# Kernel optimization log

Hardware: AMD Instinct MI355X
Metric: run time of the kernel (lower is better)

## Reference

```python
import jax, jax.numpy as jnp
import numpy as np

E = 1024   # embed_dim
H = 16     # num_heads
D = E // H # head dim = 64
NUM_BUCKETS = 32
MAX_DISTANCE = 128


def _relative_position_bucket(rel, num_buckets=NUM_BUCKETS, max_distance=MAX_DISTANCE):
    # T5-style bucketing (bidirectional): sign half + log-spaced far buckets.
    nb = num_buckets // 2
    buckets = (rel > 0).astype(jnp.int32) * nb
    rel = jnp.abs(rel)
    max_exact = nb // 2
    is_small = rel < max_exact
    # clamp to >=1 before log to avoid -inf on the masked-out branch
    rel_f = jnp.maximum(rel, 1).astype(jnp.float32)
    large = max_exact + (
        jnp.log(rel_f / max_exact) / np.log(max_distance / max_exact) * (nb - max_exact)
    ).astype(jnp.int32)
    large = jnp.minimum(large, nb - 1)
    return buckets + jnp.where(is_small, rel, large)


def setup_inputs() -> dict:
    key = jax.random.key(0)
    ks = jax.random.split(key, 6)
    B, S, K = 2, 2048, 2048
    w = 0.02
    return {
        "hidden_states": jax.random.normal(ks[0], (B, S, E), jnp.float32),
        "key_value_states": jax.random.normal(ks[1], (B, K, E), jnp.float32),
        "Wq": jax.random.normal(ks[2], (E, E), jnp.float32) * w,
        "Wkv": jax.random.normal(ks[3], (E, 2 * E), jnp.float32) * w,
        "Wo": jax.random.normal(ks[4], (E, E), jnp.float32) * w,
        "rel_bias": jax.random.normal(ks[5], (NUM_BUCKETS, H), jnp.float32) * w,
    }


def reference(hidden_states, key_value_states, Wq, Wkv, Wo, rel_bias):
    B, S, _ = hidden_states.shape
    K = key_value_states.shape[1]
    # projections (no bias, no 1/sqrt(d) scaling — T5 style)
    q = (hidden_states @ Wq).reshape(B, S, H, D).transpose(0, 2, 1, 3)      # [B,H,S,D]
    kv = (key_value_states @ Wkv).reshape(B, K, 2, H, D)
    k = kv[:, :, 0].transpose(0, 2, 1, 3)                                   # [B,H,K,D]
    v = kv[:, :, 1].transpose(0, 2, 1, 3)                                   # [B,H,K,D]
    scores = jnp.einsum('bhsd,bhkd->bhsk', q, k)                            # [B,H,S,K]
    # relative position bias
    rel = jnp.arange(K)[None, :] - jnp.arange(S)[:, None]                   # [S,K]
    buckets = _relative_position_bucket(rel)                                # [S,K]
    bias = rel_bias[buckets].transpose(2, 0, 1)[None]                       # [1,H,S,K]
    scores = scores + bias
    attn = jax.nn.softmax(scores.astype(jnp.float32), axis=-1).astype(scores.dtype)
    out = jnp.einsum('bhsk,bhkd->bshd', attn, v).reshape(B, S, E)
    return out @ Wo
```

## Files before the change

### kernel.cpp

```cpp
#include <hip/hip_runtime.h>
#include <hip/hip_bf16.h>
#include <math.h>

typedef __hip_bfloat16 bf16;
typedef __bf16 bf16x4 __attribute__((ext_vector_type(4)));
typedef __bf16 bf16x8 __attribute__((ext_vector_type(8)));
typedef float f32x4 __attribute__((ext_vector_type(4)));
typedef float f32x16 __attribute__((ext_vector_type(16)));
typedef unsigned short us4 __attribute__((ext_vector_type(4)));

#define LOG2E 1.44269504088896340736f

#if defined(__has_builtin)
#if __has_builtin(__builtin_amdgcn_exp2f)
#define EXP2(x) __builtin_amdgcn_exp2f(x)
#else
#define EXP2(x) exp2f(x)
#endif
#else
#define EXP2(x) exp2f(x)
#endif

__device__ inline __bf16 f2b(float f) {
  __hip_bfloat16 h = __float2bfloat16(f);
  return *reinterpret_cast<__bf16*>(&h);
}
__device__ inline unsigned short b2u(float f) {
  __hip_bfloat16 h = __float2bfloat16(f);
  return *reinterpret_cast<unsigned short*>(&h);
}
__device__ inline unsigned short b2u_fast(float f) {
  union { float f; unsigned u; } v;
  v.f = f;
  return (unsigned short)((v.u + 0x8000u) >> 16);
}
__device__ inline bf16x8 ld16(const bf16* p) {
  bf16x4 lo = *(const bf16x4*)p;
  bf16x4 hi = *(const bf16x4*)(p + 4);
  return __builtin_shufflevector(lo, hi, 0, 1, 2, 3, 4, 5, 6, 7);
}
__device__ inline void st16(bf16* p, uint4 v) {
  *(uint2*)p = make_uint2(v.x, v.y);
  *(uint2*)(p + 4) = make_uint2(v.z, v.w);
}
__device__ inline us4 shfl32_us4(us4 v) {
  uint2 u = *(uint2*)&v;
  u.x = __shfl_xor(u.x, 32);
  u.y = __shfl_xor(u.y, 32);
  return *(us4*)&u;
}
__device__ inline bf16x8 mk8(us4 lo, us4 hi) {
  bf16x4 l = *(bf16x4*)&lo;
  bf16x4 h = *(bf16x4*)&hi;
  return __builtin_shufflevector(l, h, 0, 1, 2, 3, 4, 5, 6, 7);
}
__device__ inline void async16(const bf16* g, bf16* l) {
  __builtin_amdgcn_global_load_lds(
      (const __attribute__((address_space(1))) unsigned int*)g,
      (__attribute__((address_space(3))) unsigned int*)l, 16, 0, 0);
}

__global__ void prep_k(const float* __restrict__ Wq, const float* __restrict__ Wkv,
                       const float* __restrict__ Wo, const float* __restrict__ rel_bias,
                       bf16* __restrict__ WqT, bf16* __restrict__ WkvT,
                       bf16* __restrict__ WoT, float* __restrict__ lut) {
  __shared__ float tile[32][33];
  int z = blockIdx.z;
  int tx = threadIdx.x, ty = threadIdx.y;
  if (z == 3) {
    if (blockIdx.y != 0 || blockIdx.x >= 16) return;
    int r = blockIdx.x * 256 + ty * 32 + tx;
    int rel = r - 2048;
    int bkt = rel > 0 ? 16 : 0;
    int ar = rel < 0 ? -rel : rel;
    int idx;
    if (ar < 8) {
      idx = bkt + ar;
    } else {
      double t = log((double)ar / 8.0) / log(16.0) * 8.0;
      int lg = 8 + (int)t;
      if (lg > 15) lg = 15;
      idx = bkt + lg;
    }
    for (int h = 0; h < 16; ++h)
      lut[h * 4096 + r] = rel_bias[idx * 16 + h] * LOG2E;
    return;
  }
  const float* in = z == 0 ? Wq : (z == 1 ? Wkv : Wo);
  bf16* out = z == 0 ? WqT : (z == 1 ? WkvT : WoT);
  int cols = z == 1 ? 2048 : 1024;
  int c0 = blockIdx.x * 32;
  if (c0 >= cols) return;
  int r0 = blockIdx.y * 32;
  for (int i = ty; i < 32; i += 8)
    tile[i][tx] = in[(size_t)(r0 + i) * cols + c0 + tx];
  __syncthreads();
  for (int i = ty; i < 32; i += 8)
    out[(size_t)(c0 + i) * 1024 + r0 + tx] = __float2bfloat16(tile[tx][i]);
}

__global__ __launch_bounds__(256) void gemm_qkv_k(const float* __restrict__ hf,
                                                  const float* __restrict__ kvf,
                                                  const bf16* __restrict__ WqT,
                                                  const bf16* __restrict__ WkvT,
                                                  bf16* __restrict__ Qb,
                                                  bf16* __restrict__ Kb,
                                                  bf16* __restrict__ Vt) {
  __shared__ __align__(16) bf16 As[128 * 32];
  __shared__ __align__(16) bf16 Bs[128 * 32];
  const int tid = threadIdx.x;
  const int lane = tid & 63;
  const int w = tid >> 6;
  const int wm = (w >> 1) * 64;
  const int wn = (w & 1) * 64;
  const int l15 = lane & 15;
  const int quad = lane >> 4;
  const int srow = lane >> 2;
  const int skg = lane & 3;

  const bool isQ = blockIdx.y < 8;
  const float* A = isQ ? hf : kvf;
  const bf16* Bt = isQ ? WqT : WkvT;
  const int n0 = (isQ ? blockIdx.y : blockIdx.y - 8) * 128;
  const int m0 = blockIdx.x * 128;
  const bool isV = (!isQ) && (n0 >= 1024);

  f32x4 acc[4][4];
#pragma unroll
  for (int i = 0; i < 4; ++i)
#pragma unroll
    for (int j = 0; j < 4; ++j) acc[i][j] = (f32x4){0.f, 0.f, 0.f, 0.f};

  for (int k0 = 0; k0 < 1024; k0 += 32) {
    __syncthreads();
#pragma unroll
    for (int rep = 0; rep < 2; ++rep) {
      int seg = w * 2 + rep;
      const float* src = A + (size_t)(m0 + seg * 16 + srow) * 1024 + k0 + skg * 8;
      float4 a0 = *(const float4*)src;
      float4 a1 = *(const float4*)(src + 4);
      bf16x8 v;
      v[0] = f2b(a0.x); v[1] = f2b(a0.y); v[2] = f2b(a0.z); v[3] = f2b(a0.w);
      v[4] = f2b(a1.x); v[5] = f2b(a1.y); v[6] = f2b(a1.z); v[7] = f2b(a1.w);
      st16(As + seg * 512 + lane * 8, *(uint4*)&v);
      async16(Bt + (size_t)(n0 + seg * 16 + srow) * 1024 + k0 + skg * 8, Bs + seg * 512);
    }
    __syncthreads();
    bf16x8 af[4], bfr[4];
#pragma unroll
    for (int i = 0; i < 4; ++i)
      af[i] = *(const bf16x8*)(As + (wm + i * 16 + l15) * 32 + quad * 8);
#pragma unroll
    for (int j = 0; j < 4; ++j)
      bfr[j] = *(const bf16x8*)(Bs + (wn + j * 16 + l15) * 32 + quad * 8);
    if (isV) {
#pragma unroll
      for (int i = 0; i < 4; ++i)
#pragma unroll
        for (int j = 0; j < 4; ++j)
          acc[i][j] = __builtin_amdgcn_mfma_f32_16x16x32_bf16(af[i], bfr[j], acc[i][j], 0, 0, 0);
    } else {
#pragma unroll
      for (int i = 0; i < 4; ++i)
#pragma unroll
        for (int j = 0; j < 4; ++j)
          acc[i][j] = __builtin_amdgcn_mfma_f32_16x16x32_bf16(bfr[j], af[i], acc[i][j], 0, 0, 0);
    }
  }

  if (isV) {
#pragma unroll
    for (int i = 0; i < 4; ++i) {
      int gmb = m0 + wm + i * 16 + quad * 4;
      int b = gmb >> 11, kp = gmb & 2047;
#pragma unroll
      for (int j = 0; j < 4; ++j) {
        int gn = n0 + wn + j * 16 + l15;
        int h = (gn >> 6) & 15, d = gn & 63;
        us4 pk;
#pragma unroll
        for (int r = 0; r < 4; ++r) pk[r] = b2u(acc[i][j][r]);
        *(us4*)(Vt + ((((size_t)b * 16 + h) * 64 + d) << 11) + kp) = pk;
      }
    }
    return;
  }
  const float scale = isQ ? LOG2E : 1.0f;
  bf16* dst = isQ ? Qb : Kb;
#pragma unroll
  for (int i = 0; i < 4; ++i) {
    int gm = m0 + wm + i * 16 + l15;
    int b = gm >> 11, s = gm & 2047;
#pragma unroll
    for (int j = 0; j < 4; ++j) {
      int gn = n0 + wn + j * 16 + quad * 4;
      int h = (gn >> 6) & 15, d0 = gn & 63;
      us4 pk;
#pragma unroll
      for (int r = 0; r < 4; ++r) pk[r] = b2u(acc[i][j][r] * scale);
      *(us4*)(dst + ((((size_t)b * 16 + h) * 2048 + s) << 6) + d0) = pk;
    }
  }
}

__global__ __launch_bounds__(256) void gemm_o_k(const bf16* __restrict__ A,
                                                const bf16* __restrict__ Bt,
                                                float* __restrict__ C0) {
  __shared__ __align__(16) bf16 As[128 * 32];
  __shared__ __align__(16) bf16 Bs[64 * 32];
  const int tid = threadIdx.x;
  const int lane = tid & 63;
  const int w = tid >> 6;
  const int wm = w * 32;
  const int m0 = blockIdx.x * 128;
  const int n0 = blockIdx.y * 64;
  const int l15 = lane & 15;
  const int quad = lane >> 4;
  const int srow = lane >> 2;
  const int skg = lane & 3;

  f32x4 acc[2][4];
#pragma unroll
  for (int i = 0; i < 2; ++i)
#pragma unroll
    for (int j = 0; j < 4; ++j) acc[i][j] = (f32x4){0.f, 0.f, 0.f, 0.f};

  for (int k0 = 0; k0 < 1024; k0 += 32) {
    __syncthreads();
#pragma unroll
    for (int rep = 0; rep < 2; ++rep) {
      int seg = w * 2 + rep;
      async16(A + (size_t)(m0 + seg * 16 + srow) * 1024 + k0 + skg * 8, As + seg * 512);
    }
    async16(Bt + (size_t)(n0 + w * 16 + srow) * 1024 + k0 + skg * 8, Bs + w * 512);
    __syncthreads();
    bf16x8 af[2], bfr[4];
#pragma unroll
    for (int i = 0; i < 2; ++i)
      af[i] = *(const bf16x8*)(As + (wm + i * 16 + l15) * 32 + quad * 8);
#pragma unroll
    for (int j = 0; j < 4; ++j)
      bfr[j] = *(const bf16x8*)(Bs + (j * 16 + l15) * 32 + quad * 8);
#pragma unroll
    for (int i = 0; i < 2; ++i)
#pragma unroll
      for (int j = 0; j < 4; ++j)
        acc[i][j] = __builtin_amdgcn_mfma_f32_16x16x32_bf16(bfr[j], af[i], acc[i][j], 0, 0, 0);
  }
#pragma unroll
  for (int i = 0; i < 2; ++i) {
    int gm = m0 + wm + i * 16 + l15;
#pragma unroll
    for (int j = 0; j < 4; ++j) {
      int gn = n0 + j * 16 + quad * 4;
      *(f32x4*)(C0 + (size_t)gm * 1024 + gn) = acc[i][j];
    }
  }
}

#define STK 68
#define SVK 136
#define KS_OFF 8704
#define VS_OFF 43520
__global__ __launch_bounds__(512, 4) void attn_k(const bf16* __restrict__ Qb,
                                                 const bf16* __restrict__ Kb,
                                                 const bf16* __restrict__ Vt,
                                                 const float* __restrict__ lut,
                                                 bf16* __restrict__ Ob) {
  __shared__ __align__(16) char smem[78336];
  float* lbias = (float*)smem;
  bf16* Ksb = (bf16*)(smem + KS_OFF);
  bf16* Vsb = (bf16*)(smem + VS_OFF);

  const int tid = threadIdx.x;
  const int lane = tid & 63;
  const int w = tid >> 6;
  const int wq = w & 3;
  const int kg = w >> 2;
  const int t256 = tid & 255;
  const int q31 = lane & 31;
  const int half = lane >> 5;

  bf16* Ks = Ksb + kg * (128 * STK);
  bf16* Vs = Vsb + kg * (64 * SVK);

  const int qt = blockIdx.x;
  const int bh = blockIdx.y;
  const int h = bh & 15, b = bh >> 4;
  const int qb = qt * 128;

  const int gbase = h * 4096 + 1921 - qb;
  for (int t = tid; t < 2175; t += 512) lbias[t] = lut[gbase + t];

  const size_t base = (size_t)bh * 2048 * 64;
  const size_t vbase = (size_t)bh * 64 * 2048;
  const int qg = qb + wq * 32 + q31;

  bf16x8 qf[4];
#pragma unroll
  for (int c = 0; c < 4; ++c)
    qf[c] = *(const bf16x8*)(Qb + base + (size_t)qg * 64 + c * 16 + half * 8);

  f32x16 oacc[2];
#pragma unroll
  for (int dj = 0; dj < 2; ++dj)
#pragma unroll
    for (int r = 0; r < 16; ++r) oacc[dj][r] = 0.f;
  float l_run = 0.f;

  const int kt0 = kg * 128;

  for (int it = 0; it < 8; ++it) {
    const int kt = it * 256 + kt0;
    __syncthreads();
    {
      uint4 kr[4], vr[4];
#pragma unroll
      for (int rep = 0; rep < 4; ++rep) {
        int slot = t256 + rep * 256;
        kr[rep] = *(const uint4*)(Kb + base + (size_t)(kt + (slot >> 3)) * 64 + (slot & 7) * 8);
        vr[rep] = *(const uint4*)(Vt + vbase + (size_t)(slot >> 4) * 2048 + kt + (slot & 15) * 8);
      }
#pragma unroll
      for (int rep = 0; rep < 4; ++rep) {
        int slot = t256 + rep * 256;
        st16(Ks + (slot >> 3) * STK + (slot & 7) * 8, kr[rep]);
        st16(Vs + (slot >> 4) * SVK + (slot & 15) * 8, vr[rep]);
      }
    }
    __syncthreads();

    const int xbase = kt + 127 + 4 * half - wq * 32 - q31;
#pragma unroll
    for (int mt = 0; mt < 4; ++mt) {
      f32x16 sacc;
#pragma unroll
      for (int a2 = 0; a2 < 4; ++a2)
#pragma unroll
        for (int rr = 0; rr < 4; ++rr)
          sacc[4 * a2 + rr] = lbias[xbase + mt * 32 + 8 * a2 + rr];
#pragma unroll
      for (int c = 0; c < 4; ++c) {
        bf16x8 kf = ld16(Ks + (mt * 32 + q31) * STK + c * 16 + half * 8);
        sacc = __builtin_amdgcn_mfma_f32_32x32x16_bf16(kf, qf[c], sacc, 0, 0, 0);
      }

      us4 ownq[4];
      f32x4 sv = (f32x4){0.f, 0.f, 0.f, 0.f};
#pragma unroll
      for (int a = 0; a < 4; ++a) {
        us4 pk;
#pragma unroll
        for (int rr = 0; rr < 4; ++rr) {
          float p = EXP2(sacc[4 * a + rr]);
          sv[rr] += p;
          pk[rr] = b2u_fast(p);
        }
        ownq[a] = pk;
      }
      l_run += (sv[0] + sv[1]) + (sv[2] + sv[3]);

      us4 rcv0 = shfl32_us4(half ? ownq[0] : ownq[1]);
      us4 rcv1 = shfl32_us4(half ? ownq[2] : ownq[3]);

#pragma unroll
      for (int p = 0; p < 2; ++p) {
        us4 rc = p ? rcv1 : rcv0;
        bf16x8 pfc = half ? mk8(rc, ownq[2 * p + 1]) : mk8(ownq[2 * p], rc);
#pragma unroll
        for (int dj = 0; dj < 2; ++dj) {
          bf16x8 vf = ld16(Vs + (dj * 32 + q31) * SVK + (mt * 2 + p) * 16 + half * 8);
          oacc[dj] = __builtin_amdgcn_mfma_f32_32x32x16_bf16(vf, pfc, oacc[dj], 0, 0, 0);
        }
      }
    }
  }

  l_run += __shfl_xor(l_run, 32);

  __syncthreads();
  float* mbuf = (float*)smem;
  if (kg) {
    float* p = mbuf + ((size_t)(wq * 64 + lane)) * 35;
    p[0] = l_run;
#pragma unroll
    for (int dj = 0; dj < 2; ++dj)
#pragma unroll
      for (int r = 0; r < 16; ++r) p[1 + dj * 16 + r] = oacc[dj][r];
  }
  __syncthreads();
  if (kg) return;

  const float* p = mbuf + ((size_t)(wq * 64 + lane)) * 35;
  float inv = 1.0f / (l_run + p[0]);

#pragma unroll
  for (int dj = 0; dj < 2; ++dj)
#pragma unroll
    for (int g = 0; g < 4; ++g) {
      us4 pk;
#pragma unroll
      for (int rr = 0; rr < 4; ++rr)
        pk[rr] = b2u((oacc[dj][4 * g + rr] + p[1 + dj * 16 + 4 * g + rr]) * inv);
      int d0 = dj * 32 + 8 * g + 4 * half;
      *(us4*)(Ob + ((size_t)(b * 2048 + qg)) * 1024 + h * 64 + d0) = pk;
    }
}

extern "C" void kernel_launch(void* const* d_in, const int* in_sizes, int n_in,
                              void* d_out, int out_size, void* d_ws, size_t ws_size,
                              hipStream_t stream) {
  const float* hidden = (const float*)d_in[0];
  const float* kvs    = (const float*)d_in[1];
  const float* Wq     = (const float*)d_in[2];
  const float* Wkv    = (const float*)d_in[3];
  const float* Wo     = (const float*)d_in[4];
  const float* relb   = (const float*)d_in[5];
  float* out = (float*)d_out;

  char* ws = (char*)d_ws;
  bf16* WqT  = (bf16*)(ws + (size_t)0);
  bf16* WkvT = (bf16*)(ws + ((size_t)2 << 20));
  bf16* WoT  = (bf16*)(ws + ((size_t)6 << 20));
  bf16* Ob   = (bf16*)(ws + ((size_t)8 << 20));
  bf16* Qb   = (bf16*)(ws + ((size_t)16 << 20));
  bf16* Kb   = (bf16*)(ws + ((size_t)24 << 20));
  bf16* Vt   = (bf16*)(ws + ((size_t)32 << 20));
  float* LUT = (float*)(ws + ((size_t)40 << 20));

  prep_k<<<dim3(64, 32, 4), dim3(32, 8), 0, stream>>>(Wq, Wkv, Wo, relb, WqT, WkvT, WoT, LUT);
  gemm_qkv_k<<<dim3(32, 24), 256, 0, stream>>>(hidden, kvs, WqT, WkvT, Qb, Kb, Vt);
  attn_k<<<dim3(16, 32), 512, 0, stream>>>(Qb, Kb, Vt, LUT, Ob);
  gemm_o_k<<<dim3(32, 16), 256, 0, stream>>>(Ob, WoT, out);
}
```

Measured before the change: 244.7 us.

## Register-prefetch next GEMM k-tile and pad LDS rows in projection GEMMs

Both projection GEMMs drop the direct global-to-LDS async loads. They now load the next k-slice into registers while MFMAs run on the current slice, then store it to LDS with a padded row stride of 36 to reduce bank conflicts on fragment reads. Launch bounds now request 3 blocks per SM. This software pipelining is meant to hide global latency, which the single-buffered loop previously exposed between the two syncs. In exchange it uses more registers and LDS, and the extra st16 ds writes replace the async path.

Measured after the change: 460.4 us. 1.88x slower.

```diff
diff --git a/kernel.cpp b/kernel.cpp
--- a/kernel.cpp
+++ b/kernel.cpp
@@ -53,11 +53,6 @@
   bf16x4 l = *(bf16x4*)&lo;
   bf16x4 h = *(bf16x4*)&hi;
   return __builtin_shufflevector(l, h, 0, 1, 2, 3, 4, 5, 6, 7);
-}
-__device__ inline void async16(const bf16* g, bf16* l) {
-  __builtin_amdgcn_global_load_lds(
-      (const __attribute__((address_space(1))) unsigned int*)g,
-      (__attribute__((address_space(3))) unsigned int*)l, 16, 0, 0);
 }
 
 __global__ void prep_k(const float* __restrict__ Wq, const float* __restrict__ Wkv,
@@ -99,15 +94,16 @@
     out[(size_t)(c0 + i) * 1024 + r0 + tx] = __float2bfloat16(tile[tx][i]);
 }
 
-__global__ __launch_bounds__(256) void gemm_qkv_k(const float* __restrict__ hf,
-                                                  const float* __restrict__ kvf,
-                                                  const bf16* __restrict__ WqT,
-                                                  const bf16* __restrict__ WkvT,
-                                                  bf16* __restrict__ Qb,
-                                                  bf16* __restrict__ Kb,
-                                                  bf16* __restrict__ Vt) {
-  __shared__ __align__(16) bf16 As[128 * 32];
-  __shared__ __align__(16) bf16 Bs[128 * 32];
+#define PS 36
+__global__ __launch_bounds__(256, 3) void gemm_qkv_k(const float* __restrict__ hf,
+                                                     const float* __restrict__ kvf,
+                                                     const bf16* __restrict__ WqT,
+                                                     const bf16* __restrict__ WkvT,
+                                                     bf16* __restrict__ Qb,
+                                                     bf16* __restrict__ Kb,
+                                                     bf16* __restrict__ Vt) {
+  __shared__ __align__(16) bf16 As[128 * PS];
+  __shared__ __align__(16) bf16 Bs[128 * PS];
   const int tid = threadIdx.x;
   const int lane = tid & 63;
   const int w = tid >> 6;
@@ -131,28 +127,42 @@
 #pragma unroll
     for (int j = 0; j < 4; ++j) acc[i][j] = (f32x4){0.f, 0.f, 0.f, 0.f};
 
-  for (int k0 = 0; k0 < 1024; k0 += 32) {
-    __syncthreads();
+  float4 pa[2][2];
+  uint4 pb[2];
+  auto LOAD = [&](int k0) {
 #pragma unroll
     for (int rep = 0; rep < 2; ++rep) {
       int seg = w * 2 + rep;
       const float* src = A + (size_t)(m0 + seg * 16 + srow) * 1024 + k0 + skg * 8;
-      float4 a0 = *(const float4*)src;
-      float4 a1 = *(const float4*)(src + 4);
+      pa[rep][0] = *(const float4*)src;
+      pa[rep][1] = *(const float4*)(src + 4);
+      pb[rep] = *(const uint4*)(Bt + (size_t)(n0 + seg * 16 + srow) * 1024 + k0 + skg * 8);
+    }
+  };
+  LOAD(0);
+
+  for (int k0 = 0; k0 < 1024; k0 += 32) {
+    __syncthreads();
+#pragma unroll
+    for (int rep = 0; rep < 2; ++rep) {
+      int seg = w * 2 + rep;
       bf16x8 v;
-      v[0] = f2b(a0.x); v[1] = f2b(a0.y); v[2] = f2b(a0.z); v[3] = f2b(a0.w);
-      v[4] = f2b(a1.x); v[5] = f2b(a1.y); v[6] = f2b(a1.z); v[7] = f2b(a1.w);
-      st16(As + seg * 512 + lane * 8, *(uint4*)&v);
-      async16(Bt + (size_t)(n0 + seg * 16 + srow) * 1024 + k0 + skg * 8, Bs + seg * 512);
-    }
-    __syncthreads();
+      v[0] = f2b(pa[rep][0].x); v[1] = f2b(pa[rep][0].y);
+      v[2] = f2b(pa[rep][0].z); v[3] = f2b(pa[rep][0].w);
+      v[4] = f2b(pa[rep][1].x); v[5] = f2b(pa[rep][1].y);
+      v[6] = f2b(pa[rep][1].z); v[7] = f2b(pa[rep][1].w);
+      st16(As + (seg * 16 + srow) * PS + skg * 8, *(uint4*)&v);
+      st16(Bs + (seg * 16 + srow) * PS + skg * 8, pb[rep]);
+    }
+    __syncthreads();
+    if (k0 + 32 < 1024) LOAD(k0 + 32);
     bf16x8 af[4], bfr[4];
 #pragma unroll
     for (int i = 0; i < 4; ++i)
-      af[i] = *(const bf16x8*)(As + (wm + i * 16 + l15) * 32 + quad * 8);
+      af[i] = ld16(As + (wm + i * 16 + l15) * PS + quad * 8);
 #pragma unroll
     for (int j = 0; j < 4; ++j)
-      bfr[j] = *(const bf16x8*)(Bs + (wn + j * 16 + l15) * 32 + quad * 8);
+      bfr[j] = ld16(Bs + (wn + j * 16 + l15) * PS + quad * 8);
     if (isV) {
 #pragma unroll
       for (int i = 0; i < 4; ++i)
@@ -203,11 +213,11 @@
   }
 }
 
-__global__ __launch_bounds__(256) void gemm_o_k(const bf16* __restrict__ A,
-                                                const bf16* __restrict__ Bt,
-                                                float* __restrict__ C0) {
-  __shared__ __align__(16) bf16 As[128 * 32];
-  __shared__ __align__(16) bf16 Bs[64 * 32];
+__global__ __launch_bounds__(256, 3) void gemm_o_k(const bf16* __restrict__ A,
+                                                   const bf16* __restrict__ Bt,
+                                                   float* __restrict__ C0) {
+  __shared__ __align__(16) bf16 As[128 * PS];
+  __shared__ __align__(16) bf16 Bs[64 * PS];
   const int tid = threadIdx.x;
   const int lane = tid & 63;
   const int w = tid >> 6;
@@ -225,22 +235,34 @@
 #pragma unroll
     for (int j = 0; j < 4; ++j) acc[i][j] = (f32x4){0.f, 0.f, 0.f, 0.f};
 
-  for (int k0 = 0; k0 < 1024; k0 += 32) {
-    __syncthreads();
+  uint4 pa[2], pbo;
+  auto LOAD = [&](int k0) {
 #pragma unroll
     for (int rep = 0; rep < 2; ++rep) {
       int seg = w * 2 + rep;
-      async16(A + (size_t)(m0 + seg * 16 + srow) * 1024 + k0 + skg * 8, As + seg * 512);
-    }
-    async16(Bt + (size_t)(n0 + w * 16 + srow) * 1024 + k0 + skg * 8, Bs + w * 512);
-    __syncthreads();
+      pa[rep] = *(const uint4*)(A + (size_t)(m0 + seg * 16 + srow) * 1024 + k0 + skg * 8);
+    }
+    pbo = *(const uint4*)(Bt + (size_t)(n0 + w * 16 + srow) * 1024 + k0 + skg * 8);
+  };
+  LOAD(0);
+
+  for (int k0 = 0; k0 < 1024; k0 += 32) {
+    __syncthreads();
+#pragma unroll
+    for (int rep = 0; rep < 2; ++rep) {
+      int seg = w * 2 + rep;
+      st16(As + (seg * 16 + srow) * PS + skg * 8, pa[rep]);
+    }
+    st16(Bs + (w * 16 + srow) * PS + skg * 8, pbo);
+    __syncthreads();
+    if (k0 + 32 < 1024) LOAD(k0 + 32);
     bf16x8 af[2], bfr[4];
 #pragma unroll
     for (int i = 0; i < 2; ++i)
-      af[i] = *(const bf16x8*)(As + (wm + i * 16 + l15) * 32 + quad * 8);
+      af[i] = ld16(As + (wm + i * 16 + l15) * PS + quad * 8);
 #pragma unroll
     for (int j = 0; j < 4; ++j)
-      bfr[j] = *(const bf16x8*)(Bs + (j * 16 + l15) * 32 + quad * 8);
+      bfr[j] = ld16(Bs + (j * 16 + l15) * PS + quad * 8);
 #pragma unroll
     for (int i = 0; i < 2; ++i)
 #pragma unroll
```

## Register-prefetch next K tile and pad LDS rows in projection GEMMs

Applied to the files above, without the earlier changes.

Both projection GEMMs drop the async global-to-LDS loads. Each iteration now loads the next K-slice into registers, overlapping that load with the MFMA work on the current tile, and writes it to LDS at the start of the following iteration. LDS rows are padded from 32 to 36 elements to reduce bank conflicts on the fragment reads, and launch bounds request 3 blocks per CU. The trade-off is higher register pressure, padded stores that need split 8-byte writes, and the loss of the direct-to-LDS load path.

New measurement: 427.9 us. 1.75x slower.

```diff
diff --git a/kernel.cpp b/kernel.cpp
--- a/kernel.cpp
+++ b/kernel.cpp
@@ -54,10 +54,11 @@
   bf16x4 h = *(bf16x4*)&hi;
   return __builtin_shufflevector(l, h, 0, 1, 2, 3, 4, 5, 6, 7);
 }
-__device__ inline void async16(const bf16* g, bf16* l) {
-  __builtin_amdgcn_global_load_lds(
-      (const __attribute__((address_space(1))) unsigned int*)g,
-      (__attribute__((address_space(3))) unsigned int*)l, 16, 0, 0);
+__device__ inline uint4 cvt8(float4 a0, float4 a1) {
+  bf16x8 v;
+  v[0] = f2b(a0.x); v[1] = f2b(a0.y); v[2] = f2b(a0.z); v[3] = f2b(a0.w);
+  v[4] = f2b(a1.x); v[5] = f2b(a1.y); v[6] = f2b(a1.z); v[7] = f2b(a1.w);
+  return *(uint4*)&v;
 }
 
 __global__ void prep_k(const float* __restrict__ Wq, const float* __restrict__ Wkv,
@@ -99,15 +100,16 @@
     out[(size_t)(c0 + i) * 1024 + r0 + tx] = __float2bfloat16(tile[tx][i]);
 }
 
-__global__ __launch_bounds__(256) void gemm_qkv_k(const float* __restrict__ hf,
-                                                  const float* __restrict__ kvf,
-                                                  const bf16* __restrict__ WqT,
-                                                  const bf16* __restrict__ WkvT,
-                                                  bf16* __restrict__ Qb,
-                                                  bf16* __restrict__ Kb,
-                                                  bf16* __restrict__ Vt) {
-  __shared__ __align__(16) bf16 As[128 * 32];
-  __shared__ __align__(16) bf16 Bs[128 * 32];
+#define PS 36
+__global__ __launch_bounds__(256, 3) void gemm_qkv_k(const float* __restrict__ hf,
+                                                     const float* __restrict__ kvf,
+                                                     const bf16* __restrict__ WqT,
+                                                     const bf16* __restrict__ WkvT,
+                                                     bf16* __restrict__ Qb,
+                                                     bf16* __restrict__ Kb,
+                                                     bf16* __restrict__ Vt) {
+  __shared__ __align__(16) bf16 As[128 * PS];
+  __shared__ __align__(16) bf16 Bs[128 * PS];
   const int tid = threadIdx.x;
   const int lane = tid & 63;
   const int w = tid >> 6;
@@ -131,28 +133,45 @@
 #pragma unroll
     for (int j = 0; j < 4; ++j) acc[i][j] = (f32x4){0.f, 0.f, 0.f, 0.f};
 
+  const float* aptr0 = A + (size_t)(m0 + (w * 2) * 16 + srow) * 1024 + skg * 8;
+  const float* aptr1 = aptr0 + 16 * 1024;
+  const bf16* bptr0 = Bt + (size_t)(n0 + (w * 2) * 16 + srow) * 1024 + skg * 8;
+  const bf16* bptr1 = bptr0 + 16 * 1024;
+  bf16* awr0 = As + ((w * 2) * 16 + srow) * PS + skg * 8;
+  bf16* awr1 = As + ((w * 2 + 1) * 16 + srow) * PS + skg * 8;
+  bf16* bwr0 = Bs + ((w * 2) * 16 + srow) * PS + skg * 8;
+  bf16* bwr1 = Bs + ((w * 2 + 1) * 16 + srow) * PS + skg * 8;
+
+  float4 pa0 = *(const float4*)(aptr0);
+  float4 pa1 = *(const float4*)(aptr0 + 4);
+  float4 pa2 = *(const float4*)(aptr1);
+  float4 pa3 = *(const float4*)(aptr1 + 4);
+  uint4 pb0 = *(const uint4*)(bptr0);
+  uint4 pb1 = *(const uint4*)(bptr1);
+
   for (int k0 = 0; k0 < 1024; k0 += 32) {
     __syncthreads();
-#pragma unroll
-    for (int rep = 0; rep < 2; ++rep) {
-      int seg = w * 2 + rep;
-      const float* src = A + (size_t)(m0 + seg * 16 + srow) * 1024 + k0 + skg * 8;
-      float4 a0 = *(const float4*)src;
-      float4 a1 = *(const float4*)(src + 4);
-      bf16x8 v;
-      v[0] = f2b(a0.x); v[1] = f2b(a0.y); v[2] = f2b(a0.z); v[3] = f2b(a0.w);
-      v[4] = f2b(a1.x); v[5] = f2b(a1.y); v[6] = f2b(a1.z); v[7] = f2b(a1.w);
-      st16(As + seg * 512 + lane * 8, *(uint4*)&v);
-      async16(Bt + (size_t)(n0 + seg * 16 + srow) * 1024 + k0 + skg * 8, Bs + seg * 512);
-    }
-    __syncthreads();
+    st16(awr0, cvt8(pa0, pa1));
+    st16(awr1, cvt8(pa2, pa3));
+    st16(bwr0, pb0);
+    st16(bwr1, pb1);
+    __syncthreads();
+    if (k0 + 32 < 1024) {
+      int kn = k0 + 32;
+      pa0 = *(const float4*)(aptr0 + kn);
+      pa1 = *(const float4*)(aptr0 + kn + 4);
+      pa2 = *(const float4*)(aptr1 + kn);
+      pa3 = *(const float4*)(aptr1 + kn + 4);
+      pb0 = *(const uint4*)(bptr0 + kn);
+      pb1 = *(const uint4*)(bptr1 + kn);
+    }
     bf16x8 af[4], bfr[4];
 #pragma unroll
     for (int i = 0; i < 4; ++i)
-      af[i] = *(const bf16x8*)(As + (wm + i * 16 + l15) * 32 + quad * 8);
+      af[i] = ld16(As + (wm + i * 16 + l15) * PS + quad * 8);
 #pragma unroll
     for (int j = 0; j < 4; ++j)
-      bfr[j] = *(const bf16x8*)(Bs + (wn + j * 16 + l15) * 32 + quad * 8);
+      bfr[j] = ld16(Bs + (wn + j * 16 + l15) * PS + quad * 8);
     if (isV) {
 #pragma unroll
       for (int i = 0; i < 4; ++i)
@@ -203,11 +222,11 @@
   }
 }
 
-__global__ __launch_bounds__(256) void gemm_o_k(const bf16* __restrict__ A,
-                                                const bf16* __restrict__ Bt,
-                                                float* __restrict__ C0) {
-  __shared__ __align__(16) bf16 As[128 * 32];
-  __shared__ __align__(16) bf16 Bs[64 * 32];
+__global__ __launch_bounds__(256, 3) void gemm_o_k(const bf16* __restrict__ A,
+                                                   const bf16* __restrict__ Bt,
+                                                   float* __restrict__ C0) {
+  __shared__ __align__(16) bf16 As[128 * PS];
+  __shared__ __align__(16) bf16 Bs[64 * PS];
   const int tid = threadIdx.x;
   const int lane = tid & 63;
   const int w = tid >> 6;
@@ -225,22 +244,36 @@
 #pragma unroll
     for (int j = 0; j < 4; ++j) acc[i][j] = (f32x4){0.f, 0.f, 0.f, 0.f};
 
+  const bf16* aptr0 = A + (size_t)(m0 + (w * 2) * 16 + srow) * 1024 + skg * 8;
+  const bf16* aptr1 = aptr0 + 16 * 1024;
+  const bf16* bptr = Bt + (size_t)(n0 + w * 16 + srow) * 1024 + skg * 8;
+  bf16* awr0 = As + ((w * 2) * 16 + srow) * PS + skg * 8;
+  bf16* awr1 = As + ((w * 2 + 1) * 16 + srow) * PS + skg * 8;
+  bf16* bwr = Bs + (w * 16 + srow) * PS + skg * 8;
+
+  uint4 po0 = *(const uint4*)(aptr0);
+  uint4 po1 = *(const uint4*)(aptr1);
+  uint4 pbo = *(const uint4*)(bptr);
+
   for (int k0 = 0; k0 < 1024; k0 += 32) {
     __syncthreads();
-#pragma unroll
-    for (int rep = 0; rep < 2; ++rep) {
-      int seg = w * 2 + rep;
-      async16(A + (size_t)(m0 + seg * 16 + srow) * 1024 + k0 + skg * 8, As + seg * 512);
-    }
-    async16(Bt + (size_t)(n0 + w * 16 + srow) * 1024 + k0 + skg * 8, Bs + w * 512);
-    __syncthreads();
+    st16(awr0, po0);
+    st16(awr1, po1);
+    st16(bwr, pbo);
+    __syncthreads();
+    if (k0 + 32 < 1024) {
+      int kn = k0 + 32;
+      po0 = *(const uint4*)(aptr0 + kn);
+      po1 = *(const uint4*)(aptr1 + kn);
+      pbo = *(const uint4*)(bptr + kn);
+    }
     bf16x8 af[2], bfr[4];
 #pragma unroll
     for (int i = 0; i < 2; ++i)
-      af[i] = *(const bf16x8*)(As + (wm + i * 16 + l15) * 32 + quad * 8);
+      af[i] = ld16(As + (wm + i * 16 + l15) * PS + quad * 8);
 #pragma unroll
     for (int j = 0; j < 4; ++j)
-      bfr[j] = *(const bf16x8*)(Bs + (j * 16 + l15) * 32 + quad * 8);
+      bfr[j] = ld16(Bs + (j * 16 + l15) * PS + quad * 8);
 #pragma unroll
     for (int i = 0; i < 2; ++i)
 #pragma unroll
```

## Pre-cast activations to bf16, async-load GEMM A tiles, prefetch K/V in attention

Applied to the files above, without the earlier changes.

Adds a separate cast kernel that converts hidden and key/value states to bf16 once, staging them in the Ob workspace and in the output buffer. The QKV GEMM can then load its A tiles straight into LDS asynchronously instead of converting fp32 per tile. The attention kernel now prefetches the next K/V tile into registers while the current one is being computed, and its launch bound drops from 4 to 2 waves per SIMD to leave room for the extra registers. This costs an extra kernel launch and a round trip through memory for the bf16 copies, and the lower occupancy could hurt latency hiding.

New measurement: 226.9 us. 7.3% less time.

```diff
diff --git a/kernel.cpp b/kernel.cpp
--- a/kernel.cpp
+++ b/kernel.cpp
@@ -21,6 +21,7 @@
 #define EXP2(x) exp2f(x)
 #endif
 
+
 __device__ inline __bf16 f2b(float f) {
   __hip_bfloat16 h = __float2bfloat16(f);
   return *reinterpret_cast<__bf16*>(&h);
@@ -58,6 +59,20 @@
   __builtin_amdgcn_global_load_lds(
       (const __attribute__((address_space(1))) unsigned int*)g,
       (__attribute__((address_space(3))) unsigned int*)l, 16, 0, 0);
+}
+
+__global__ void cast2_k(const float* __restrict__ a, const float* __restrict__ b,
+                        bf16* __restrict__ oa, bf16* __restrict__ ob) {
+  int gid = blockIdx.x * 256 + threadIdx.x;
+  const float* in = (gid < 524288) ? a : b;
+  bf16* out = (gid < 524288) ? oa : ob;
+  int i = (gid & 524287) * 8;
+  float4 a0 = *(const float4*)(in + i);
+  float4 a1 = *(const float4*)(in + i + 4);
+  bf16x8 v;
+  v[0] = f2b(a0.x); v[1] = f2b(a0.y); v[2] = f2b(a0.z); v[3] = f2b(a0.w);
+  v[4] = f2b(a1.x); v[5] = f2b(a1.y); v[6] = f2b(a1.z); v[7] = f2b(a1.w);
+  *(bf16x8*)(out + i) = v;
 }
 
 __global__ void prep_k(const float* __restrict__ Wq, const float* __restrict__ Wkv,
@@ -99,8 +114,8 @@
     out[(size_t)(c0 + i) * 1024 + r0 + tx] = __float2bfloat16(tile[tx][i]);
 }
 
-__global__ __launch_bounds__(256) void gemm_qkv_k(const float* __restrict__ hf,
-                                                  const float* __restrict__ kvf,
+__global__ __launch_bounds__(256) void gemm_qkv_k(const bf16* __restrict__ hbf,
+                                                  const bf16* __restrict__ kbf,
                                                   const bf16* __restrict__ WqT,
                                                   const bf16* __restrict__ WkvT,
                                                   bf16* __restrict__ Qb,
@@ -119,7 +134,7 @@
   const int skg = lane & 3;
 
   const bool isQ = blockIdx.y < 8;
-  const float* A = isQ ? hf : kvf;
+  const bf16* A = isQ ? hbf : kbf;
   const bf16* Bt = isQ ? WqT : WkvT;
   const int n0 = (isQ ? blockIdx.y : blockIdx.y - 8) * 128;
   const int m0 = blockIdx.x * 128;
@@ -136,13 +151,7 @@
 #pragma unroll
     for (int rep = 0; rep < 2; ++rep) {
       int seg = w * 2 + rep;
-      const float* src = A + (size_t)(m0 + seg * 16 + srow) * 1024 + k0 + skg * 8;
-      float4 a0 = *(const float4*)src;
-      float4 a1 = *(const float4*)(src + 4);
-      bf16x8 v;
-      v[0] = f2b(a0.x); v[1] = f2b(a0.y); v[2] = f2b(a0.z); v[3] = f2b(a0.w);
-      v[4] = f2b(a1.x); v[5] = f2b(a1.y); v[6] = f2b(a1.z); v[7] = f2b(a1.w);
-      st16(As + seg * 512 + lane * 8, *(uint4*)&v);
+      async16(A + (size_t)(m0 + seg * 16 + srow) * 1024 + k0 + skg * 8, As + seg * 512);
       async16(Bt + (size_t)(n0 + seg * 16 + srow) * 1024 + k0 + skg * 8, Bs + seg * 512);
     }
     __syncthreads();
@@ -262,7 +271,7 @@
 #define SVK 136
 #define KS_OFF 8704
 #define VS_OFF 43520
-__global__ __launch_bounds__(512, 4) void attn_k(const bf16* __restrict__ Qb,
+__global__ __launch_bounds__(512, 2) void attn_k(const bf16* __restrict__ Qb,
                                                  const bf16* __restrict__ Kb,
                                                  const bf16* __restrict__ Vt,
                                                  const float* __restrict__ lut,
@@ -310,25 +319,33 @@
 
   const int kt0 = kg * 128;
 
+  uint4 kr[4], vr[4];
+#pragma unroll
+  for (int rep = 0; rep < 4; ++rep) {
+    int slot = t256 + rep * 256;
+    kr[rep] = *(const uint4*)(Kb + base + (size_t)(kt0 + (slot >> 3)) * 64 + (slot & 7) * 8);
+    vr[rep] = *(const uint4*)(Vt + vbase + (size_t)(slot >> 4) * 2048 + kt0 + (slot & 15) * 8);
+  }
+
   for (int it = 0; it < 8; ++it) {
     const int kt = it * 256 + kt0;
     __syncthreads();
-    {
-      uint4 kr[4], vr[4];
+#pragma unroll
+    for (int rep = 0; rep < 4; ++rep) {
+      int slot = t256 + rep * 256;
+      st16(Ks + (slot >> 3) * STK + (slot & 7) * 8, kr[rep]);
+      st16(Vs + (slot >> 4) * SVK + (slot & 15) * 8, vr[rep]);
+    }
+    __syncthreads();
+    if (it < 7) {
+      const int nkt = kt + 256;
 #pragma unroll
       for (int rep = 0; rep < 4; ++rep) {
         int slot = t256 + rep * 256;
-        kr[rep] = *(const uint4*)(Kb + base + (size_t)(kt + (slot >> 3)) * 64 + (slot & 7) * 8);
-        vr[rep] = *(const uint4*)(Vt + vbase + (size_t)(slot >> 4) * 2048 + kt + (slot & 15) * 8);
+        kr[rep] = *(const uint4*)(Kb + base + (size_t)(nkt + (slot >> 3)) * 64 + (slot & 7) * 8);
+        vr[rep] = *(const uint4*)(Vt + vbase + (size_t)(slot >> 4) * 2048 + nkt + (slot & 15) * 8);
       }
-#pragma unroll
-      for (int rep = 0; rep < 4; ++rep) {
-        int slot = t256 + rep * 256;
-        st16(Ks + (slot >> 3) * STK + (slot & 7) * 8, kr[rep]);
-        st16(Vs + (slot >> 4) * SVK + (slot & 15) * 8, vr[rep]);
-      }
-    }
-    __syncthreads();
+    }
 
     const int xbase = kt + 127 + 4 * half - wq * 32 - q31;
 #pragma unroll
@@ -423,13 +440,16 @@
   bf16* WkvT = (bf16*)(ws + ((size_t)2 << 20));
   bf16* WoT  = (bf16*)(ws + ((size_t)6 << 20));
   bf16* Ob   = (bf16*)(ws + ((size_t)8 << 20));
+  bf16* hbf  = Ob;
   bf16* Qb   = (bf16*)(ws + ((size_t)16 << 20));
   bf16* Kb   = (bf16*)(ws + ((size_t)24 << 20));
   bf16* Vt   = (bf16*)(ws + ((size_t)32 << 20));
   float* LUT = (float*)(ws + ((size_t)40 << 20));
+  bf16* kbf  = (bf16*)d_out;
 
   prep_k<<<dim3(64, 32, 4), dim3(32, 8), 0, stream>>>(Wq, Wkv, Wo, relb, WqT, WkvT, WoT, LUT);
-  gemm_qkv_k<<<dim3(32, 24), 256, 0, stream>>>(hidden, kvs, WqT, WkvT, Qb, Kb, Vt);
+  cast2_k<<<4096, 256, 0, stream>>>(hidden, kvs, hbf, kbf);
+  gemm_qkv_k<<<dim3(32, 24), 256, 0, stream>>>(hbf, kbf, WqT, WkvT, Qb, Kb, Vt);
   attn_k<<<dim3(16, 32), 512, 0, stream>>>(Qb, Kb, Vt, LUT, Ob);
   gemm_o_k<<<dim3(32, 16), 256, 0, stream>>>(Ob, WoT, out);
 }
```
